# Kernel optimization log

Measured on AMD Instinct MI355X. Metric: run time of the kernel, lower is better.

## Reference

```python
import jax, jax.numpy as jnp
import numpy as np

N = 50000          # nodes
E = 800000         # edges (avg degree 16)
FEATS = [96, 96, 96, 48]


def setup_inputs() -> dict:
    key = jax.random.key(0)
    ks = jax.random.split(key, 10)
    x = jax.random.normal(ks[0], (N, FEATS[0]), dtype=jnp.float32)
    edge_index = jax.random.randint(ks[1], (2, E), 0, N, dtype=jnp.int64)
    d = {"x": x, "edge_index": edge_index}
    i = 2
    for l in range(3):
        s = 1.0 / np.sqrt(FEATS[l])
        d[f"Wl{l}"] = jax.random.uniform(ks[i], (FEATS[l], FEATS[l + 1]), jnp.float32, -s, s); i += 1
        d[f"Wr{l}"] = jax.random.uniform(ks[i], (FEATS[l], FEATS[l + 1]), jnp.float32, -s, s); i += 1
        d[f"b{l}"] = jnp.zeros((FEATS[l + 1],), jnp.float32)
    return d


def _sage_layer(h, src, dst, Wl, Wr, b, n):
    # PyG SAGEConv (aggr='mean', root_weight=True, normalize=False):
    # out_i = W_l @ mean_{j in N(i)} h_j + W_r @ h_i + b
    msg = h[src]                                                   # [E, F] gather
    ssum = jax.ops.segment_sum(msg, dst, num_segments=n)           # [N, F] scatter-add
    cnt = jax.ops.segment_sum(jnp.ones((src.shape[0], 1), h.dtype), dst, num_segments=n)
    mean = ssum / jnp.maximum(cnt, 1.0)
    return mean @ Wl + h @ Wr + b


def reference(x, edge_index, Wl0, Wr0, b0, Wl1, Wr1, b1, Wl2, Wr2, b2):
    src, dst = edge_index[0], edge_index[1]
    n = x.shape[0]
    # block = SAGEConv -> ReLU -> dropout(identity in eval)
    h = jax.nn.relu(_sage_layer(x, src, dst, Wl0, Wr0, b0, n))
    h = jax.nn.relu(_sage_layer(h, src, dst, Wl1, Wr1, b1, n))
    h = jax.nn.relu(_sage_layer(h, src, dst, Wl2, Wr2, b2, n))
    return h
```

## Files before the change

kernel.cpp:

```cpp
#include <hip/hip_runtime.h>


#define NNODES 50000
#define ZROW   50000
#define NEDGES 800000
#define CAP    64
#define EB 3125
#define CVT_N8 600000
#define CB 2344
#define WTN 46080
#define WB 180

typedef __attribute__((ext_vector_type(8))) short bf16x8;
typedef __attribute__((ext_vector_type(4))) float f32x4;

__device__ inline unsigned short f2bf(float f) {
    unsigned int u = __float_as_uint(f);
    unsigned int r = (u + 0x7fffu + ((u >> 16) & 1u)) >> 16;
    return (unsigned short)r;
}
__device__ inline float bf2f_lo(unsigned int u) { return __uint_as_float(u << 16); }
__device__ inline float bf2f_hi(unsigned int u) { return __uint_as_float(u & 0xffff0000u); }

__global__ void build_cvt(const int* __restrict__ src, const int* __restrict__ dst,
                          int* __restrict__ deg, int* __restrict__ col,
                          const float* __restrict__ x, unsigned short* __restrict__ h0b,
                          unsigned short* __restrict__ h1b, unsigned short* __restrict__ h2b,
                          const float* __restrict__ Wl0, const float* __restrict__ Wr0,
                          const float* __restrict__ Wl1, const float* __restrict__ Wr1,
                          const float* __restrict__ Wl2, const float* __restrict__ Wr2,
                          unsigned short* __restrict__ WT0, unsigned short* __restrict__ WT1,
                          unsigned short* __restrict__ WT2) {
    int b = blockIdx.x;
    if (b < EB) {
        int e = b * 256 + threadIdx.x;
        int d = dst[e];
        int r = atomicAdd(&deg[d], 1);
        if (r < CAP) col[(size_t)d * CAP + r] = src[e];
    } else if (b < EB + CB) {
        long long t = (long long)(b - EB) * 256 + threadIdx.x;
        if (t < CVT_N8) {
            const float4* p = reinterpret_cast<const float4*>(x + t * 8);
            float4 a = p[0], c = p[1];
            uint4 o;
            o.x = (unsigned)f2bf(a.x) | ((unsigned)f2bf(a.y) << 16);
            o.y = (unsigned)f2bf(a.z) | ((unsigned)f2bf(a.w) << 16);
            o.z = (unsigned)f2bf(c.x) | ((unsigned)f2bf(c.y) << 16);
            o.w = (unsigned)f2bf(c.z) | ((unsigned)f2bf(c.w) << 16);
            *reinterpret_cast<uint4*>(h0b + t * 8) = o;
        }
    } else if (b < EB + CB + WB) {
        int t = (b - EB - CB) * 256 + threadIdx.x;
        if (t >= WTN) return;
        const float* Wl; const float* Wr; unsigned short* WT; int fout; int u;
        if (t < 18432)      { Wl = Wl0; Wr = Wr0; WT = WT0; fout = 96; u = t; }
        else if (t < 36864) { Wl = Wl1; Wr = Wr1; WT = WT1; fout = 96; u = t - 18432; }
        else                { Wl = Wl2; Wr = Wr2; WT = WT2; fout = 48; u = t - 36864; }
        int j = u / 192;
        int k = u - j * 192;
        float v = (k < 96) ? Wl[k * fout + j] : Wr[(k - 96) * fout + j];
        WT[u] = f2bf(v);
    } else {
        int t = threadIdx.x;
        if (t < 36) {
            uint4 z = make_uint4(0, 0, 0, 0);
            unsigned short* base = (t < 12) ? h0b : (t < 24) ? h1b : h2b;
            int c = (t % 12) * 8;
            *reinterpret_cast<uint4*>(base + (size_t)ZROW * 96 + c) = z;
        }
    }
}

template <int NT, bool WRITE_BF16>
__global__ __launch_bounds__(256) void fused_layer(
    const unsigned short* __restrict__ hb,
    const int* __restrict__ deg, const int* __restrict__ col,
    const unsigned short* __restrict__ WT,
    const float* __restrict__ bias,
    unsigned short* __restrict__ out_bf, float* __restrict__ out_f) {
    __shared__ unsigned short Asm[16][200];
    __shared__ int cols[16 * CAP];
    const int i0 = blockIdx.x * 16;
    const int t = threadIdx.x;

    {
        int q = t * 4;
        int node = q >> 6;
        int slot = q & 63;
        int4 v = *reinterpret_cast<const int4*>(col + (size_t)i0 * CAP + q);
        int d = deg[i0 + node];
        v.x = (slot + 0 < d) ? v.x : ZROW;
        v.y = (slot + 1 < d) ? v.y : ZROW;
        v.z = (slot + 2 < d) ? v.z : ZROW;
        v.w = (slot + 3 < d) ? v.w : ZROW;
        *reinterpret_cast<int4*>(&cols[q]) = v;
    }
    __syncthreads();

    if (t < 192) {
        const int nl = t / 12;
        const int c = (t - nl * 12) * 8;
        const int d = deg[i0 + nl];
        const int pd = (d + 7) & ~7;
        float a0 = 0.f, a1 = 0.f, a2 = 0.f, a3 = 0.f, a4 = 0.f, a5 = 0.f, a6 = 0.f, a7 = 0.f;
        for (int j = 0; j < pd; j += 8) {
            int4 ca = *reinterpret_cast<const int4*>(&cols[nl * CAP + j]);
            int4 cb = *reinterpret_cast<const int4*>(&cols[nl * CAP + j + 4]);
            uint4 u0 = *reinterpret_cast<const uint4*>(hb + (size_t)ca.x * 96 + c);
            uint4 u1 = *reinterpret_cast<const uint4*>(hb + (size_t)ca.y * 96 + c);
            uint4 u2 = *reinterpret_cast<const uint4*>(hb + (size_t)ca.z * 96 + c);
            uint4 u3 = *reinterpret_cast<const uint4*>(hb + (size_t)ca.w * 96 + c);
            uint4 u4 = *reinterpret_cast<const uint4*>(hb + (size_t)cb.x * 96 + c);
            uint4 u5 = *reinterpret_cast<const uint4*>(hb + (size_t)cb.y * 96 + c);
            uint4 u6 = *reinterpret_cast<const uint4*>(hb + (size_t)cb.z * 96 + c);
            uint4 u7 = *reinterpret_cast<const uint4*>(hb + (size_t)cb.w * 96 + c);
            a0 += bf2f_lo(u0.x) + bf2f_lo(u1.x) + bf2f_lo(u2.x) + bf2f_lo(u3.x)
                + bf2f_lo(u4.x) + bf2f_lo(u5.x) + bf2f_lo(u6.x) + bf2f_lo(u7.x);
            a1 += bf2f_hi(u0.x) + bf2f_hi(u1.x) + bf2f_hi(u2.x) + bf2f_hi(u3.x)
                + bf2f_hi(u4.x) + bf2f_hi(u5.x) + bf2f_hi(u6.x) + bf2f_hi(u7.x);
            a2 += bf2f_lo(u0.y) + bf2f_lo(u1.y) + bf2f_lo(u2.y) + bf2f_lo(u3.y)
                + bf2f_lo(u4.y) + bf2f_lo(u5.y) + bf2f_lo(u6.y) + bf2f_lo(u7.y);
            a3 += bf2f_hi(u0.y) + bf2f_hi(u1.y) + bf2f_hi(u2.y) + bf2f_hi(u3.y)
                + bf2f_hi(u4.y) + bf2f_hi(u5.y) + bf2f_hi(u6.y) + bf2f_hi(u7.y);
            a4 += bf2f_lo(u0.z) + bf2f_lo(u1.z) + bf2f_lo(u2.z) + bf2f_lo(u3.z)
                + bf2f_lo(u4.z) + bf2f_lo(u5.z) + bf2f_lo(u6.z) + bf2f_lo(u7.z);
            a5 += bf2f_hi(u0.z) + bf2f_hi(u1.z) + bf2f_hi(u2.z) + bf2f_hi(u3.z)
                + bf2f_hi(u4.z) + bf2f_hi(u5.z) + bf2f_hi(u6.z) + bf2f_hi(u7.z);
            a6 += bf2f_lo(u0.w) + bf2f_lo(u1.w) + bf2f_lo(u2.w) + bf2f_lo(u3.w)
                + bf2f_lo(u4.w) + bf2f_lo(u5.w) + bf2f_lo(u6.w) + bf2f_lo(u7.w);
            a7 += bf2f_hi(u0.w) + bf2f_hi(u1.w) + bf2f_hi(u2.w) + bf2f_hi(u3.w)
                + bf2f_hi(u4.w) + bf2f_hi(u5.w) + bf2f_hi(u6.w) + bf2f_hi(u7.w);
        }
        float inv = (d > 0) ? 1.0f / (float)d : 0.0f;
        uint4 o;
        o.x = (unsigned)f2bf(a0 * inv) | ((unsigned)f2bf(a1 * inv) << 16);
        o.y = (unsigned)f2bf(a2 * inv) | ((unsigned)f2bf(a3 * inv) << 16);
        o.z = (unsigned)f2bf(a4 * inv) | ((unsigned)f2bf(a5 * inv) << 16);
        o.w = (unsigned)f2bf(a6 * inv) | ((unsigned)f2bf(a7 * inv) << 16);
        *reinterpret_cast<uint4*>(&Asm[nl][c]) = o;
    }
    __syncthreads();

    const int wave = t >> 6;
    const int lane = t & 63;
    if (wave >= NT) return;
    const int m = lane & 15;
    const int kq = (lane >> 4) * 8;

    bf16x8 afr[6];
#pragma unroll
    for (int kk = 0; kk < 3; ++kk)
        afr[kk] = *reinterpret_cast<const bf16x8*>(&Asm[m][kq + kk * 32]);
    const unsigned short* hrow = hb + (size_t)(i0 + m) * 96 + kq;
#pragma unroll
    for (int kk = 0; kk < 3; ++kk)
        afr[3 + kk] = *reinterpret_cast<const bf16x8*>(hrow + kk * 32);

    const int r0 = (lane >> 4) * 4;
    for (int nt = wave; nt < NT; nt += 4) {
        f32x4 acc = {0.f, 0.f, 0.f, 0.f};
        const unsigned short* wrow = WT + (size_t)(nt * 16 + m) * 192 + kq;
#pragma unroll
        for (int kk = 0; kk < 6; ++kk) {
            bf16x8 bfr = *reinterpret_cast<const bf16x8*>(wrow + kk * 32);
            acc = __builtin_amdgcn_mfma_f32_16x16x32_bf16(afr[kk], bfr, acc, 0, 0, 0);
        }
        int colj = nt * 16 + m;
        float bv = bias[colj];
#pragma unroll
        for (int r = 0; r < 4; ++r) {
            float v = fmaxf(acc[r] + bv, 0.0f);
            size_t oi = (size_t)(i0 + r0 + r) * (16 * NT) + colj;
            if (WRITE_BF16) out_bf[oi] = f2bf(v);
            else            out_f[oi] = v;
        }
    }
}

extern "C" void kernel_launch(void* const* d_in, const int* in_sizes, int n_in,
                              void* d_out, int out_size, void* d_ws, size_t ws_size,
                              hipStream_t stream) {
    const float* x   = (const float*)d_in[0];
    const int*   ei  = (const int*)d_in[1];
    const float* Wl0 = (const float*)d_in[2];
    const float* Wr0 = (const float*)d_in[3];
    const float* b0  = (const float*)d_in[4];
    const float* Wl1 = (const float*)d_in[5];
    const float* Wr1 = (const float*)d_in[6];
    const float* b1  = (const float*)d_in[7];
    const float* Wl2 = (const float*)d_in[8];
    const float* Wr2 = (const float*)d_in[9];
    const float* b2  = (const float*)d_in[10];
    float* out = (float*)d_out;

    const int* src = ei;
    const int* dst = ei + NEDGES;

    char* p = (char*)d_ws;
    int* deg = (int*)p;                  p += 50176 * 4;
    int* col = (int*)p;                  p += (size_t)NNODES * CAP * 4;
    unsigned short* WT0 = (unsigned short*)p; p += 96 * 192 * 2;
    unsigned short* WT1 = (unsigned short*)p; p += 96 * 192 * 2;
    unsigned short* WT2 = (unsigned short*)p; p += 48 * 192 * 2;
    unsigned short* h0b = (unsigned short*)p; p += (size_t)(NNODES + 1) * 96 * 2;
    unsigned short* h1b = (unsigned short*)p; p += (size_t)(NNODES + 1) * 96 * 2;
    unsigned short* h2b = (unsigned short*)p; p += (size_t)(NNODES + 1) * 96 * 2;

    hipMemsetAsync(deg, 0, NNODES * sizeof(int), stream);
    build_cvt<<<EB + CB + WB + 1, 256, 0, stream>>>(
        src, dst, deg, col, x, h0b, h1b, h2b,
        Wl0, Wr0, Wl1, Wr1, Wl2, Wr2, WT0, WT1, WT2);

    const int LB = NNODES / 16;
    fused_layer<6, true><<<LB, 256, 0, stream>>>(h0b, deg, col, WT0, b0, h1b, nullptr);
    fused_layer<6, true><<<LB, 256, 0, stream>>>(h1b, deg, col, WT1, b1, h2b, nullptr);
    fused_layer<3, false><<<LB, 256, 0, stream>>>(h2b, deg, col, WT2, b2, nullptr, out);
}
```

Baseline: 225.7 us.

## Process 32 nodes per 384-thread block so all threads gather and all waves run MFMA

Each block now covers 32 nodes with 384 threads instead of 16 nodes with 256 threads. All threads take part in the neighbor gather, where previously 64 sat idle, and the six waves split into two 16-row M tiles that each cover three N tiles in an unrolled loop. The shared column buffer gets a padded stride to reduce LDS bank conflicts, and buffers are padded to 50176 rows with bounds checks on the last partial block. The intent is less thread idling and fewer blocks, at the cost of more LDS and registers per block, which may lower occupancy.

```diff
diff --git a/kernel.cpp b/kernel.cpp
--- a/kernel.cpp
+++ b/kernel.cpp
@@ -2,9 +2,11 @@
 
 
 #define NNODES 50000
+#define NPAD   50176
 #define ZROW   50000
 #define NEDGES 800000
 #define CAP    64
+#define CSTR   68
 #define EB 3125
 #define CVT_N8 600000
 #define CB 2344
@@ -72,40 +74,40 @@
 }
 
 template <int NT, bool WRITE_BF16>
-__global__ __launch_bounds__(256) void fused_layer(
+__global__ __launch_bounds__(384) void fused_layer(
     const unsigned short* __restrict__ hb,
     const int* __restrict__ deg, const int* __restrict__ col,
     const unsigned short* __restrict__ WT,
     const float* __restrict__ bias,
     unsigned short* __restrict__ out_bf, float* __restrict__ out_f) {
-    __shared__ unsigned short Asm[16][200];
-    __shared__ int cols[16 * CAP];
-    const int i0 = blockIdx.x * 16;
+    __shared__ unsigned short Asm[32][200];
+    __shared__ int cols[32 * CSTR];
+    const int i0 = blockIdx.x * 32;
     const int t = threadIdx.x;
 
-    {
-        int q = t * 4;
+    for (int q = t * 4; q < 32 * CAP; q += 384 * 4) {
         int node = q >> 6;
         int slot = q & 63;
-        int4 v = *reinterpret_cast<const int4*>(col + (size_t)i0 * CAP + q);
+        int4 v = *reinterpret_cast<const int4*>(col + (size_t)(i0 + node) * CAP + slot);
         int d = deg[i0 + node];
         v.x = (slot + 0 < d) ? v.x : ZROW;
         v.y = (slot + 1 < d) ? v.y : ZROW;
         v.z = (slot + 2 < d) ? v.z : ZROW;
         v.w = (slot + 3 < d) ? v.w : ZROW;
-        *reinterpret_cast<int4*>(&cols[q]) = v;
+        *reinterpret_cast<int4*>(&cols[node * CSTR + slot]) = v;
     }
     __syncthreads();
 
-    if (t < 192) {
+    {
         const int nl = t / 12;
         const int c = (t - nl * 12) * 8;
-        const int d = deg[i0 + nl];
+        const int node = i0 + nl;
+        const int d = (node < NNODES) ? deg[node] : 0;
         const int pd = (d + 7) & ~7;
         float a0 = 0.f, a1 = 0.f, a2 = 0.f, a3 = 0.f, a4 = 0.f, a5 = 0.f, a6 = 0.f, a7 = 0.f;
         for (int j = 0; j < pd; j += 8) {
-            int4 ca = *reinterpret_cast<const int4*>(&cols[nl * CAP + j]);
-            int4 cb = *reinterpret_cast<const int4*>(&cols[nl * CAP + j + 4]);
+            int4 ca = *reinterpret_cast<const int4*>(&cols[nl * CSTR + j]);
+            int4 cb = *reinterpret_cast<const int4*>(&cols[nl * CSTR + j + 4]);
             uint4 u0 = *reinterpret_cast<const uint4*>(hb + (size_t)ca.x * 96 + c);
             uint4 u1 = *reinterpret_cast<const uint4*>(hb + (size_t)ca.y * 96 + c);
             uint4 u2 = *reinterpret_cast<const uint4*>(hb + (size_t)ca.z * 96 + c);
@@ -143,21 +145,26 @@
 
     const int wave = t >> 6;
     const int lane = t & 63;
-    if (wave >= NT) return;
+    const int mt = (wave >= 3) ? 1 : 0;
+    const int w3 = wave - mt * 3;
     const int m = lane & 15;
     const int kq = (lane >> 4) * 8;
+    const int row0 = i0 + mt * 16;
 
     bf16x8 afr[6];
 #pragma unroll
     for (int kk = 0; kk < 3; ++kk)
-        afr[kk] = *reinterpret_cast<const bf16x8*>(&Asm[m][kq + kk * 32]);
-    const unsigned short* hrow = hb + (size_t)(i0 + m) * 96 + kq;
+        afr[kk] = *reinterpret_cast<const bf16x8*>(&Asm[mt * 16 + m][kq + kk * 32]);
+    const unsigned short* hrow = hb + (size_t)(row0 + m) * 96 + kq;
 #pragma unroll
     for (int kk = 0; kk < 3; ++kk)
         afr[3 + kk] = *reinterpret_cast<const bf16x8*>(hrow + kk * 32);
 
     const int r0 = (lane >> 4) * 4;
-    for (int nt = wave; nt < NT; nt += 4) {
+    constexpr int REP = (NT + 2) / 3;
+#pragma unroll
+    for (int rep = 0; rep < REP; ++rep) {
+        int nt = w3 + rep * 3;
         f32x4 acc = {0.f, 0.f, 0.f, 0.f};
         const unsigned short* wrow = WT + (size_t)(nt * 16 + m) * 192 + kq;
 #pragma unroll
@@ -170,9 +177,12 @@
 #pragma unroll
         for (int r = 0; r < 4; ++r) {
             float v = fmaxf(acc[r] + bv, 0.0f);
-            size_t oi = (size_t)(i0 + r0 + r) * (16 * NT) + colj;
-            if (WRITE_BF16) out_bf[oi] = f2bf(v);
-            else            out_f[oi] = v;
+            int row = row0 + r0 + r;
+            if (row < NNODES) {
+                size_t oi = (size_t)row * (16 * NT) + colj;
+                if (WRITE_BF16) out_bf[oi] = f2bf(v);
+                else            out_f[oi] = v;
+            }
         }
     }
 }
@@ -197,22 +207,22 @@
     const int* dst = ei + NEDGES;
 
     char* p = (char*)d_ws;
-    int* deg = (int*)p;                  p += 50176 * 4;
-    int* col = (int*)p;                  p += (size_t)NNODES * CAP * 4;
+    int* deg = (int*)p;                  p += (size_t)NPAD * 4;
+    int* col = (int*)p;                  p += (size_t)NPAD * CAP * 4;
     unsigned short* WT0 = (unsigned short*)p; p += 96 * 192 * 2;
     unsigned short* WT1 = (unsigned short*)p; p += 96 * 192 * 2;
     unsigned short* WT2 = (unsigned short*)p; p += 48 * 192 * 2;
-    unsigned short* h0b = (unsigned short*)p; p += (size_t)(NNODES + 1) * 96 * 2;
-    unsigned short* h1b = (unsigned short*)p; p += (size_t)(NNODES + 1) * 96 * 2;
-    unsigned short* h2b = (unsigned short*)p; p += (size_t)(NNODES + 1) * 96 * 2;
-
-    hipMemsetAsync(deg, 0, NNODES * sizeof(int), stream);
+    unsigned short* h0b = (unsigned short*)p; p += (size_t)NPAD * 96 * 2;
+    unsigned short* h1b = (unsigned short*)p; p += (size_t)NPAD * 96 * 2;
+    unsigned short* h2b = (unsigned short*)p; p += (size_t)NPAD * 96 * 2;
+
+    hipMemsetAsync(deg, 0, (size_t)NPAD * sizeof(int), stream);
     build_cvt<<<EB + CB + WB + 1, 256, 0, stream>>>(
         src, dst, deg, col, x, h0b, h1b, h2b,
         Wl0, Wr0, Wl1, Wr1, Wl2, Wr2, WT0, WT1, WT2);
 
-    const int LB = NNODES / 16;
-    fused_layer<6, true><<<LB, 256, 0, stream>>>(h0b, deg, col, WT0, b0, h1b, nullptr);
-    fused_layer<6, true><<<LB, 256, 0, stream>>>(h1b, deg, col, WT1, b1, h2b, nullptr);
-    fused_layer<3, false><<<LB, 256, 0, stream>>>(h2b, deg, col, WT2, b2, nullptr, out);
-}
+    const int LB = (NNODES + 31) / 32;
+    fused_layer<6, true><<<LB, 384, 0, stream>>>(h0b, deg, col, WT0, b0, h1b, nullptr);
+    fused_layer<6, true><<<LB, 384, 0, stream>>>(h1b, deg, col, WT1, b1, h2b, nullptr);
+    fused_layer<3, false><<<LB, 384, 0, stream>>>(h2b, deg, col, WT2, b2, nullptr, out);
+}
```

Result: slower. 247.6 us (+9.7%).

## Split node features into 32-column planes and parallelize neighbor gather across 16 lanes

Applied to the files above, without the earlier changes.

Node features are stored as three planar 32-column bf16 slabs instead of 96-wide rows, so each plane is a smaller working set that fits cache better during the gather. The aggregation now uses all 256 threads, 16 per node, with four lanes splitting the neighbor list and combining partial sums via shuffles, where before only 192 threads each walked all neighbors. The cols shared array is padded to reduce bank conflicts. In exchange, each block makes three passes over the neighbor list, adds shuffle reductions, and writes outputs scattered across planes.

```diff
diff --git a/kernel.cpp b/kernel.cpp
--- a/kernel.cpp
+++ b/kernel.cpp
@@ -2,9 +2,12 @@
 
 
 #define NNODES 50000
+#define NPAD   50176
 #define ZROW   50000
 #define NEDGES 800000
 #define CAP    64
+#define CSTR   68
+#define PL     ((size_t)NPAD * 32)
 #define EB 3125
 #define CVT_N8 600000
 #define CB 2344
@@ -40,14 +43,18 @@
     } else if (b < EB + CB) {
         long long t = (long long)(b - EB) * 256 + threadIdx.x;
         if (t < CVT_N8) {
-            const float4* p = reinterpret_cast<const float4*>(x + t * 8);
-            float4 a = p[0], c = p[1];
+            int n = (int)(t / 12);
+            int c = (int)(t - (long long)n * 12);
+            int pp = c >> 2;
+            int c4 = c & 3;
+            const float4* p4 = reinterpret_cast<const float4*>(x + (size_t)n * 96 + c * 8);
+            float4 a = p4[0], cc = p4[1];
             uint4 o;
             o.x = (unsigned)f2bf(a.x) | ((unsigned)f2bf(a.y) << 16);
             o.y = (unsigned)f2bf(a.z) | ((unsigned)f2bf(a.w) << 16);
-            o.z = (unsigned)f2bf(c.x) | ((unsigned)f2bf(c.y) << 16);
-            o.w = (unsigned)f2bf(c.z) | ((unsigned)f2bf(c.w) << 16);
-            *reinterpret_cast<uint4*>(h0b + t * 8) = o;
+            o.z = (unsigned)f2bf(cc.x) | ((unsigned)f2bf(cc.y) << 16);
+            o.w = (unsigned)f2bf(cc.z) | ((unsigned)f2bf(cc.w) << 16);
+            *reinterpret_cast<uint4*>(h0b + (size_t)pp * PL + (size_t)n * 32 + c4 * 8) = o;
         }
     } else if (b < EB + CB + WB) {
         int t = (b - EB - CB) * 256 + threadIdx.x;
@@ -65,8 +72,10 @@
         if (t < 36) {
             uint4 z = make_uint4(0, 0, 0, 0);
             unsigned short* base = (t < 12) ? h0b : (t < 24) ? h1b : h2b;
-            int c = (t % 12) * 8;
-            *reinterpret_cast<uint4*>(base + (size_t)ZROW * 96 + c) = z;
+            int u = t % 12;
+            int pp = u >> 2;
+            int s = u & 3;
+            *reinterpret_cast<uint4*>(base + (size_t)pp * PL + (size_t)ZROW * 32 + s * 8) = z;
         }
     }
 }
@@ -77,9 +86,10 @@
     const int* __restrict__ deg, const int* __restrict__ col,
     const unsigned short* __restrict__ WT,
     const float* __restrict__ bias,
-    unsigned short* __restrict__ out_bf, float* __restrict__ out_f) {
+    unsigned short* __restrict__ out_bf,
+    float* __restrict__ out_f) {
     __shared__ unsigned short Asm[16][200];
-    __shared__ int cols[16 * CAP];
+    __shared__ int cols[16 * CSTR];
     const int i0 = blockIdx.x * 16;
     const int t = threadIdx.x;
 
@@ -87,63 +97,81 @@
         int q = t * 4;
         int node = q >> 6;
         int slot = q & 63;
-        int4 v = *reinterpret_cast<const int4*>(col + (size_t)i0 * CAP + q);
+        int4 v = *reinterpret_cast<const int4*>(col + (size_t)(i0 + node) * CAP + slot);
         int d = deg[i0 + node];
         v.x = (slot + 0 < d) ? v.x : ZROW;
         v.y = (slot + 1 < d) ? v.y : ZROW;
         v.z = (slot + 2 < d) ? v.z : ZROW;
         v.w = (slot + 3 < d) ? v.w : ZROW;
-        *reinterpret_cast<int4*>(&cols[q]) = v;
+        *reinterpret_cast<int4*>(&cols[node * CSTR + slot]) = v;
     }
     __syncthreads();
 
-    if (t < 192) {
-        const int nl = t / 12;
-        const int c = (t - nl * 12) * 8;
-        const int d = deg[i0 + nl];
+    {
+        const int node = t >> 4;
+        const int r = t & 15;
+        const int c4 = r & 3;
+        const int q = r >> 2;
+        const int coff = c4 * 8;
+        const int d = deg[i0 + node];
         const int pd = (d + 7) & ~7;
-        float a0 = 0.f, a1 = 0.f, a2 = 0.f, a3 = 0.f, a4 = 0.f, a5 = 0.f, a6 = 0.f, a7 = 0.f;
-        for (int j = 0; j < pd; j += 8) {
-            int4 ca = *reinterpret_cast<const int4*>(&cols[nl * CAP + j]);
-            int4 cb = *reinterpret_cast<const int4*>(&cols[nl * CAP + j + 4]);
-            uint4 u0 = *reinterpret_cast<const uint4*>(hb + (size_t)ca.x * 96 + c);
-            uint4 u1 = *reinterpret_cast<const uint4*>(hb + (size_t)ca.y * 96 + c);
-            uint4 u2 = *reinterpret_cast<const uint4*>(hb + (size_t)ca.z * 96 + c);
-            uint4 u3 = *reinterpret_cast<const uint4*>(hb + (size_t)ca.w * 96 + c);
-            uint4 u4 = *reinterpret_cast<const uint4*>(hb + (size_t)cb.x * 96 + c);
-            uint4 u5 = *reinterpret_cast<const uint4*>(hb + (size_t)cb.y * 96 + c);
-            uint4 u6 = *reinterpret_cast<const uint4*>(hb + (size_t)cb.z * 96 + c);
-            uint4 u7 = *reinterpret_cast<const uint4*>(hb + (size_t)cb.w * 96 + c);
-            a0 += bf2f_lo(u0.x) + bf2f_lo(u1.x) + bf2f_lo(u2.x) + bf2f_lo(u3.x)
-                + bf2f_lo(u4.x) + bf2f_lo(u5.x) + bf2f_lo(u6.x) + bf2f_lo(u7.x);
-            a1 += bf2f_hi(u0.x) + bf2f_hi(u1.x) + bf2f_hi(u2.x) + bf2f_hi(u3.x)
-                + bf2f_hi(u4.x) + bf2f_hi(u5.x) + bf2f_hi(u6.x) + bf2f_hi(u7.x);
-            a2 += bf2f_lo(u0.y) + bf2f_lo(u1.y) + bf2f_lo(u2.y) + bf2f_lo(u3.y)
-                + bf2f_lo(u4.y) + bf2f_lo(u5.y) + bf2f_lo(u6.y) + bf2f_lo(u7.y);
-            a3 += bf2f_hi(u0.y) + bf2f_hi(u1.y) + bf2f_hi(u2.y) + bf2f_hi(u3.y)
-                + bf2f_hi(u4.y) + bf2f_hi(u5.y) + bf2f_hi(u6.y) + bf2f_hi(u7.y);
-            a4 += bf2f_lo(u0.z) + bf2f_lo(u1.z) + bf2f_lo(u2.z) + bf2f_lo(u3.z)
-                + bf2f_lo(u4.z) + bf2f_lo(u5.z) + bf2f_lo(u6.z) + bf2f_lo(u7.z);
-            a5 += bf2f_hi(u0.z) + bf2f_hi(u1.z) + bf2f_hi(u2.z) + bf2f_hi(u3.z)
-                + bf2f_hi(u4.z) + bf2f_hi(u5.z) + bf2f_hi(u6.z) + bf2f_hi(u7.z);
-            a6 += bf2f_lo(u0.w) + bf2f_lo(u1.w) + bf2f_lo(u2.w) + bf2f_lo(u3.w)
-                + bf2f_lo(u4.w) + bf2f_lo(u5.w) + bf2f_lo(u6.w) + bf2f_lo(u7.w);
-            a7 += bf2f_hi(u0.w) + bf2f_hi(u1.w) + bf2f_hi(u2.w) + bf2f_hi(u3.w)
-                + bf2f_hi(u4.w) + bf2f_hi(u5.w) + bf2f_hi(u6.w) + bf2f_hi(u7.w);
-        }
-        float inv = (d > 0) ? 1.0f / (float)d : 0.0f;
-        uint4 o;
-        o.x = (unsigned)f2bf(a0 * inv) | ((unsigned)f2bf(a1 * inv) << 16);
-        o.y = (unsigned)f2bf(a2 * inv) | ((unsigned)f2bf(a3 * inv) << 16);
-        o.z = (unsigned)f2bf(a4 * inv) | ((unsigned)f2bf(a5 * inv) << 16);
-        o.w = (unsigned)f2bf(a6 * inv) | ((unsigned)f2bf(a7 * inv) << 16);
-        *reinterpret_cast<uint4*>(&Asm[nl][c]) = o;
+        const float inv = (d > 0) ? 1.0f / (float)d : 0.0f;
+
+#pragma unroll
+        for (int pp = 0; pp < 3; ++pp) {
+            const unsigned short* __restrict__ plane = hb + (size_t)pp * PL;
+            float a0 = 0.f, a1 = 0.f, a2 = 0.f, a3 = 0.f;
+            float a4 = 0.f, a5 = 0.f, a6 = 0.f, a7 = 0.f;
+            for (int j = q * 8; j < pd; j += 32) {
+                int4 ca = *reinterpret_cast<const int4*>(&cols[node * CSTR + j]);
+                int4 cb = *reinterpret_cast<const int4*>(&cols[node * CSTR + j + 4]);
+                uint4 u0 = *reinterpret_cast<const uint4*>(plane + (size_t)ca.x * 32 + coff);
+                uint4 u1 = *reinterpret_cast<const uint4*>(plane + (size_t)ca.y * 32 + coff);
+                uint4 u2 = *reinterpret_cast<const uint4*>(plane + (size_t)ca.z * 32 + coff);
+                uint4 u3 = *reinterpret_cast<const uint4*>(plane + (size_t)ca.w * 32 + coff);
+                uint4 u4 = *reinterpret_cast<const uint4*>(plane + (size_t)cb.x * 32 + coff);
+                uint4 u5 = *reinterpret_cast<const uint4*>(plane + (size_t)cb.y * 32 + coff);
+                uint4 u6 = *reinterpret_cast<const uint4*>(plane + (size_t)cb.z * 32 + coff);
+                uint4 u7 = *reinterpret_cast<const uint4*>(plane + (size_t)cb.w * 32 + coff);
+                a0 += bf2f_lo(u0.x) + bf2f_lo(u1.x) + bf2f_lo(u2.x) + bf2f_lo(u3.x)
+                    + bf2f_lo(u4.x) + bf2f_lo(u5.x) + bf2f_lo(u6.x) + bf2f_lo(u7.x);
+                a1 += bf2f_hi(u0.x) + bf2f_hi(u1.x) + bf2f_hi(u2.x) + bf2f_hi(u3.x)
+                    + bf2f_hi(u4.x) + bf2f_hi(u5.x) + bf2f_hi(u6.x) + bf2f_hi(u7.x);
+                a2 += bf2f_lo(u0.y) + bf2f_lo(u1.y) + bf2f_lo(u2.y) + bf2f_lo(u3.y)
+                    + bf2f_lo(u4.y) + bf2f_lo(u5.y) + bf2f_lo(u6.y) + bf2f_lo(u7.y);
+                a3 += bf2f_hi(u0.y) + bf2f_hi(u1.y) + bf2f_hi(u2.y) + bf2f_hi(u3.y)
+                    + bf2f_hi(u4.y) + bf2f_hi(u5.y) + bf2f_hi(u6.y) + bf2f_hi(u7.y);
+                a4 += bf2f_lo(u0.z) + bf2f_lo(u1.z) + bf2f_lo(u2.z) + bf2f_lo(u3.z)
+                    + bf2f_lo(u4.z) + bf2f_lo(u5.z) + bf2f_lo(u6.z) + bf2f_lo(u7.z);
+                a5 += bf2f_hi(u0.z) + bf2f_hi(u1.z) + bf2f_hi(u2.z) + bf2f_hi(u3.z)
+                    + bf2f_hi(u4.z) + bf2f_hi(u5.z) + bf2f_hi(u6.z) + bf2f_hi(u7.z);
+                a6 += bf2f_lo(u0.w) + bf2f_lo(u1.w) + bf2f_lo(u2.w) + bf2f_lo(u3.w)
+                    + bf2f_lo(u4.w) + bf2f_lo(u5.w) + bf2f_lo(u6.w) + bf2f_lo(u7.w);
+                a7 += bf2f_hi(u0.w) + bf2f_hi(u1.w) + bf2f_hi(u2.w) + bf2f_hi(u3.w)
+                    + bf2f_hi(u4.w) + bf2f_hi(u5.w) + bf2f_hi(u6.w) + bf2f_hi(u7.w);
+            }
+            a0 += __shfl_down(a0, 8); a1 += __shfl_down(a1, 8);
+            a2 += __shfl_down(a2, 8); a3 += __shfl_down(a3, 8);
+            a4 += __shfl_down(a4, 8); a5 += __shfl_down(a5, 8);
+            a6 += __shfl_down(a6, 8); a7 += __shfl_down(a7, 8);
+            a0 += __shfl_down(a0, 4); a1 += __shfl_down(a1, 4);
+            a2 += __shfl_down(a2, 4); a3 += __shfl_down(a3, 4);
+            a4 += __shfl_down(a4, 4); a5 += __shfl_down(a5, 4);
+            a6 += __shfl_down(a6, 4); a7 += __shfl_down(a7, 4);
+            if (q == 0) {
+                uint4 o;
+                o.x = (unsigned)f2bf(a0 * inv) | ((unsigned)f2bf(a1 * inv) << 16);
+                o.y = (unsigned)f2bf(a2 * inv) | ((unsigned)f2bf(a3 * inv) << 16);
+                o.z = (unsigned)f2bf(a4 * inv) | ((unsigned)f2bf(a5 * inv) << 16);
+                o.w = (unsigned)f2bf(a6 * inv) | ((unsigned)f2bf(a7 * inv) << 16);
+                *reinterpret_cast<uint4*>(&Asm[node][pp * 32 + coff]) = o;
+            }
+        }
     }
     __syncthreads();
 
     const int wave = t >> 6;
     const int lane = t & 63;
-    if (wave >= NT) return;
     const int m = lane & 15;
     const int kq = (lane >> 4) * 8;
 
@@ -151,10 +179,10 @@
 #pragma unroll
     for (int kk = 0; kk < 3; ++kk)
         afr[kk] = *reinterpret_cast<const bf16x8*>(&Asm[m][kq + kk * 32]);
-    const unsigned short* hrow = hb + (size_t)(i0 + m) * 96 + kq;
 #pragma unroll
     for (int kk = 0; kk < 3; ++kk)
-        afr[3 + kk] = *reinterpret_cast<const bf16x8*>(hrow + kk * 32);
+        afr[3 + kk] = *reinterpret_cast<const bf16x8*>(
+            hb + (size_t)kk * PL + (size_t)(i0 + m) * 32 + kq);
 
     const int r0 = (lane >> 4) * 4;
     for (int nt = wave; nt < NT; nt += 4) {
@@ -170,9 +198,12 @@
 #pragma unroll
         for (int r = 0; r < 4; ++r) {
             float v = fmaxf(acc[r] + bv, 0.0f);
-            size_t oi = (size_t)(i0 + r0 + r) * (16 * NT) + colj;
-            if (WRITE_BF16) out_bf[oi] = f2bf(v);
-            else            out_f[oi] = v;
+            int row = i0 + r0 + r;
+            if (WRITE_BF16) {
+                out_bf[(size_t)(colj >> 5) * PL + (size_t)row * 32 + (colj & 31)] = f2bf(v);
+            } else {
+                out_f[(size_t)row * (16 * NT) + colj] = v;
+            }
         }
     }
 }
@@ -197,16 +228,16 @@
     const int* dst = ei + NEDGES;
 
     char* p = (char*)d_ws;
-    int* deg = (int*)p;                  p += 50176 * 4;
-    int* col = (int*)p;                  p += (size_t)NNODES * CAP * 4;
+    int* deg = (int*)p;                  p += (size_t)NPAD * 4;
+    int* col = (int*)p;                  p += (size_t)NPAD * CAP * 4;
     unsigned short* WT0 = (unsigned short*)p; p += 96 * 192 * 2;
     unsigned short* WT1 = (unsigned short*)p; p += 96 * 192 * 2;
     unsigned short* WT2 = (unsigned short*)p; p += 48 * 192 * 2;
-    unsigned short* h0b = (unsigned short*)p; p += (size_t)(NNODES + 1) * 96 * 2;
-    unsigned short* h1b = (unsigned short*)p; p += (size_t)(NNODES + 1) * 96 * 2;
-    unsigned short* h2b = (unsigned short*)p; p += (size_t)(NNODES + 1) * 96 * 2;
-
-    hipMemsetAsync(deg, 0, NNODES * sizeof(int), stream);
+    unsigned short* h0b = (unsigned short*)p; p += 3 * PL * 2;
+    unsigned short* h1b = (unsigned short*)p; p += 3 * PL * 2;
+    unsigned short* h2b = (unsigned short*)p; p += 3 * PL * 2;
+
+    hipMemsetAsync(deg, 0, (size_t)NPAD * sizeof(int), stream);
     build_cvt<<<EB + CB + WB + 1, 256, 0, stream>>>(
         src, dst, deg, col, x, h0b, h1b, h2b,
         Wl0, Wr0, Wl1, Wr1, Wl2, Wr2, WT0, WT1, WT2);
```

New measurement: 238.9 us. 5.9% more time.
